# Kernel tuning notes

Hardware: AMD Instinct MI355X
Metric: run time of the kernel (lower is better)

The kernel has to match this reference:

```python
import jax, jax.numpy as jnp
import numpy as np

B = 4096
N_BLOCK = 100
N_SLOT = 300
N_YS = 1236
HID = 256
STEPS = 100
NEG = -1000.0


def _init_w(key, shape):
    # uniform(-1/sqrt(fan_in), 1/sqrt(fan_in)) like torch Linear/LSTMCell
    fan = shape[-1]
    return jax.random.uniform(key, shape, jnp.float32, -1.0, 1.0) / jnp.sqrt(jnp.float32(fan))


def setup_inputs() -> dict:
    key = jax.random.key(0)
    ks = jax.random.split(key, 16)
    to_tensor = jax.random.uniform(ks[0], (B, N_BLOCK, 5), jnp.float32)
    ti_tensor = jax.random.uniform(ks[1], (B, N_BLOCK, 5), jnp.float32)
    ys_tensor = jax.random.uniform(ks[2], (B, N_YS, 5), jnp.float32)
    # many slots are feasible, count starts at 5 so the decrement/zero-out logic is exercised.
    dims = jax.random.uniform(ks[3], (B, N_SLOT, 4), jnp.float32) * 2.0
    count = jnp.full((B, N_SLOT, 1), 5.0, jnp.float32)
    slot_info = jnp.concatenate([dims, count], axis=-1)
    params = dict(
        W1=_init_w(ks[4], (512, 1436)), b1=jnp.zeros(512, jnp.float32),
        W2=_init_w(ks[5], (512, 512)), b2=jnp.zeros(512, jnp.float32),
        W3=_init_w(ks[6], (256, 512)), b3=jnp.zeros(256, jnp.float32),
        W_fe2=_init_w(ks[7], (1, 5)), b_fe2=jnp.zeros(1, jnp.float32),
        Wih_to=_init_w(ks[8], (4 * HID, 5)), Whh_to=_init_w(ks[9], (4 * HID, HID)),
        bih_to=jnp.zeros(4 * HID, jnp.float32), bhh_to=jnp.zeros(4 * HID, jnp.float32),
        Wih_ti=_init_w(ks[10], (4 * HID, 5)), Whh_ti=_init_w(ks[11], (4 * HID, HID)),
        bih_ti=jnp.zeros(4 * HID, jnp.float32), bhh_ti=jnp.zeros(4 * HID, jnp.float32),
        Wb=_init_w(ks[12], (N_BLOCK, HID)), bb=jnp.zeros(N_BLOCK, jnp.float32),
        Ws=_init_w(ks[13], (N_SLOT, HID)), bs=jnp.zeros(N_SLOT, jnp.float32),
    )
    return {"to_tensor": to_tensor, "ti_tensor": ti_tensor, "ys_tensor": ys_tensor,
            "slot_info": slot_info, **params}


def _lstm(x, h, c, Wih, Whh, bih, bhh):
    g = x @ Wih.T + bih + h @ Whh.T + bhh  # [B, 4H]
    i, f, gg, o = jnp.split(g, 4, axis=-1)  # torch gate order: i, f, g, o
    c = jax.nn.sigmoid(f) * c + jax.nn.sigmoid(i) * jnp.tanh(gg)
    h = jax.nn.sigmoid(o) * jnp.tanh(c)
    return h, c


def reference(to_tensor, ti_tensor, ys_tensor, slot_info,
              W1, b1, W2, b2, W3, b3, W_fe2, b_fe2,
              Wih_to, Whh_to, bih_to, bhh_to,
              Wih_ti, Whh_ti, bih_ti, bhh_ti,
              Wb, bb, Ws, bs):
    state = jnp.concatenate([to_tensor, ti_tensor, ys_tensor], axis=1)  # [B,1436,5]
    x = state.transpose(0, 2, 1)                    # [B,5,1436]
    x = jax.nn.relu(x @ W1.T + b1)                  # Dropout is identity in eval mode
    x = jax.nn.relu(x @ W2.T + b2)
    x = jax.nn.relu(x @ W3.T + b3)                  # [B,5,256]
    feat_vec = (x.transpose(0, 2, 1) @ W_fe2.T + b_fe2)[..., 0]  # [B,256]

    bsz = to_tensor.shape[0]
    batch_idx = jnp.arange(bsz)
    zeros5 = jnp.zeros((bsz, 5), to_tensor.dtype)   # input_ti is never updated in the loop
    mask_to0 = to_tensor[:, :, 0] != -1.0
    mask_ti0 = ti_tensor[:, :, 0] != -1.0
    carry0 = (feat_vec, jnp.zeros((bsz, HID), jnp.float32),
              feat_vec, jnp.zeros((bsz, HID), jnp.float32),
              zeros5, mask_to0, mask_ti0, slot_info)

    def step(carry, _):
        h_to, c_to, h_ti, c_ti, inp_to, m_to, m_ti, slots = carry
        h_to, c_to = _lstm(inp_to, h_to, c_to, Wih_to, Whh_to, bih_to, bhh_to)
        # masked block logits; argmax of softmax == argmax of masked logits
        logit_b = jnp.where(m_to, h_to @ Wb.T + bb, NEG)
        sel_b = jnp.argmax(logit_b, axis=-1)                      # [B]
        inp_to = jnp.take_along_axis(to_tensor, sel_b[:, None, None], axis=1)[:, 0, :]  # [B,5]
        m_to = m_to.at[batch_idx, sel_b].set(False)
        # slot feasibility: block (l,w) must be strictly smaller than slot (l,w), slot nonempty
        slot_mask = jnp.any(inp_to[:, None, :2] >= slots[:, :, :2], axis=-1) | (slots[:, :, 0] == 0.0)
        logit_s = jnp.where(slot_mask, NEG, h_to @ Ws.T + bs)
        sel_s = jnp.argmax(logit_s, axis=-1)
        slots = slots.at[batch_idx, sel_s, 4].add(-1.0)
        slots = jnp.where((slots[:, :, 4] == 0.0)[:, :, None], 0.0, slots)
        h_ti, c_ti = _lstm(zeros5, h_ti, c_ti, Wih_ti, Whh_ti, bih_ti, bhh_ti)
        logit_bti = jnp.where(m_ti, h_ti @ Wb.T + bb, NEG)
        sel_bti = jnp.argmax(logit_bti, axis=-1)
        m_ti = m_ti.at[batch_idx, sel_bti].set(False)
        out = jnp.stack([sel_b, sel_s, sel_bti], axis=-1)         # [B,3]
        return (h_to, c_to, h_ti, c_ti, inp_to, m_to, m_ti, slots), out

    _, acts = jax.lax.scan(step, carry0, None, length=STEPS)      # [100,B,3]
    actions = acts.transpose(1, 0, 2)                             # [B,100,3]
    return state, actions
```

## Files before the change

### kernel.cpp

```cpp
#include <hip/hip_runtime.h>
#include <cstddef>

#define BATCH   4096
#define NBLK    100
#define NSLOT   300
#define NSTATE  1436
#define HID     256
#define NSTEPS  100
#define NEGV    (-1000.0f)
#define KC      384


__device__ __forceinline__ float sigf(float x) {
#pragma clang fp contract(off)
  float e = (float)exp(-(double)x);
  float d = 1.0f + e;
  return 1.0f / d;
}
__device__ __forceinline__ float tanhf32(float x) {
  return (float)tanh((double)x);
}

__device__ __forceinline__ void argmax64f(float& v, int& i) {
#pragma unroll
  for (int off = 32; off > 0; off >>= 1) {
    float v2 = __shfl_down(v, off, 64);
    int   i2 = __shfl_down(i, off, 64);
    if (v2 > v || (v2 == v && i2 < i)) { v = v2; i = i2; }
  }
  v = __shfl(v, 0, 64);
  i = __shfl(i, 0, 64);
}

__global__ __launch_bounds__(256) void concat_kernel(
    const float* __restrict__ to_t, const float* __restrict__ ti_t,
    const float* __restrict__ ys_t, float* __restrict__ state)
{
  int b = blockIdx.x;
  for (int li = threadIdx.x; li < 7180; li += 256) {
    float v = (li < 500)  ? to_t[(size_t)b * 500 + li]
            : (li < 1000) ? ti_t[(size_t)b * 500 + (li - 500)]
                          : ys_t[(size_t)b * 6180 + (li - 1000)];
    state[(size_t)b * 7180 + li] = v;
  }
}

__device__ __forceinline__ void gemm32_tile(
    const float* __restrict__ A, int lda,
    const float* __restrict__ W, int ldw,
    const float* __restrict__ bias,
    float* __restrict__ C, int ldc,
    int N, int K, int row0, int col0, bool relu)
{
#pragma clang fp contract(off)
  __shared__ float As[16][68];
  __shared__ float Ws[16][68];
  const int t = threadIdx.x;
  const int tx = t & 15, ty = t >> 4;
  const int mload = t >> 2;
  const int kq    = (t & 3) << 2;
  const int gn    = col0 + mload;
  const float* Aptr = A + (size_t)(row0 + mload) * lda + kq;
  const float* Wptr = (gn < N) ? (W + (size_t)gn * ldw + kq) : nullptr;

  float acc[4][4] = {};
  float res[4][4];
  bool first = true;
  for (int k0 = 0; k0 < K; k0 += 16) {
    if (k0 > 0 && (k0 % KC) == 0) {
#pragma unroll
      for (int i = 0; i < 4; i++)
#pragma unroll
        for (int j = 0; j < 4; j++) {
          res[i][j] = first ? acc[i][j] : (res[i][j] + acc[i][j]);
          acc[i][j] = 0.0f;
        }
      first = false;
    }
    float4 av = *(const float4*)(Aptr + k0);
    float4 wv = make_float4(0.f, 0.f, 0.f, 0.f);
    if (Wptr) wv = *(const float4*)(Wptr + k0);
    As[kq + 0][mload] = av.x; As[kq + 1][mload] = av.y;
    As[kq + 2][mload] = av.z; As[kq + 3][mload] = av.w;
    Ws[kq + 0][mload] = wv.x; Ws[kq + 1][mload] = wv.y;
    Ws[kq + 2][mload] = wv.z; Ws[kq + 3][mload] = wv.w;
    __syncthreads();
#pragma unroll
    for (int kk = 0; kk < 16; kk++) {
      float a[4], w[4];
#pragma unroll
      for (int i = 0; i < 4; i++) { a[i] = As[kk][ty * 4 + i]; w[i] = Ws[kk][tx * 4 + i]; }
#pragma unroll
      for (int i = 0; i < 4; i++)
#pragma unroll
        for (int j = 0; j < 4; j++) acc[i][j] = fmaf(a[i], w[j], acc[i][j]);
    }
    __syncthreads();
  }
#pragma unroll
  for (int i = 0; i < 4; i++)
#pragma unroll
    for (int j = 0; j < 4; j++)
      res[i][j] = first ? acc[i][j] : (res[i][j] + acc[i][j]);

#pragma unroll
  for (int i = 0; i < 4; i++) {
    size_t row = (size_t)(row0 + ty * 4 + i) * ldc;
#pragma unroll
    for (int j = 0; j < 4; j++) {
      int n = col0 + tx * 4 + j;
      if (n < N) {
        float v = res[i][j] + bias[n];
        if (relu) v = v > 0.0f ? v : 0.0f;
        C[row + n] = v;
      }
    }
  }
}

__global__ __launch_bounds__(256) void gemm32_kernel(
    const float* __restrict__ A, int lda, const float* __restrict__ W, int ldw,
    const float* __restrict__ bias, float* __restrict__ C, int ldc,
    int N, int K, int relu)
{
  gemm32_tile(A, lda, W, ldw, bias, C, ldc, N, K,
              blockIdx.y * 64, blockIdx.x * 64, relu != 0);
}

__global__ __launch_bounds__(256) void gemm1_kernel(
    const float* __restrict__ state, const float* __restrict__ W1,
    const float* __restrict__ b1, float* __restrict__ X1, int row_base)
{
#pragma clang fp contract(off)
  __shared__ float As[16][68];
  __shared__ float Ws[16][68];
  const int t = threadIdx.x;
  const int tx = t & 15, ty = t >> 4;
  const int mload = t >> 2;
  const int kq    = (t & 3) << 2;
  const int row0 = blockIdx.y * 64, col0 = blockIdx.x * 64;
  const int R = row_base + row0 + mload;
  const int b = R / 5, j = R - b * 5;
  const float* sp = state + (size_t)b * 7180 + j;
  const float* Wptr = W1 + (size_t)(col0 + mload) * NSTATE + kq;

  float acc[4][4] = {};
  float res[4][4];
  bool first = true;
  for (int k0 = 0; k0 < 1440; k0 += 16) {
    if (k0 == 384 || k0 == 768 || k0 == 1152) {
#pragma unroll
      for (int i = 0; i < 4; i++)
#pragma unroll
        for (int jj = 0; jj < 4; jj++) {
          res[i][jj] = first ? acc[i][jj] : (res[i][jj] + acc[i][jj]);
          acc[i][jj] = 0.0f;
        }
      first = false;
    }
    int n = k0 + kq;
    float a0 = (n + 0 < NSTATE) ? sp[(n + 0) * 5] : 0.0f;
    float a1 = (n + 1 < NSTATE) ? sp[(n + 1) * 5] : 0.0f;
    float a2 = (n + 2 < NSTATE) ? sp[(n + 2) * 5] : 0.0f;
    float a3 = (n + 3 < NSTATE) ? sp[(n + 3) * 5] : 0.0f;
    float4 wv = make_float4(0.f, 0.f, 0.f, 0.f);
    if (n + 3 < NSTATE) wv = *(const float4*)(Wptr + k0);
    As[kq + 0][mload] = a0; As[kq + 1][mload] = a1;
    As[kq + 2][mload] = a2; As[kq + 3][mload] = a3;
    Ws[kq + 0][mload] = wv.x; Ws[kq + 1][mload] = wv.y;
    Ws[kq + 2][mload] = wv.z; Ws[kq + 3][mload] = wv.w;
    __syncthreads();
#pragma unroll
    for (int kk = 0; kk < 16; kk++) {
      float a[4], w[4];
#pragma unroll
      for (int i = 0; i < 4; i++) { a[i] = As[kk][ty * 4 + i]; w[i] = Ws[kk][tx * 4 + i]; }
#pragma unroll
      for (int i = 0; i < 4; i++)
#pragma unroll
        for (int jj = 0; jj < 4; jj++) acc[i][jj] = fmaf(a[i], w[jj], acc[i][jj]);
    }
    __syncthreads();
  }
#pragma unroll
  for (int i = 0; i < 4; i++)
#pragma unroll
    for (int jj = 0; jj < 4; jj++)
      res[i][jj] = res[i][jj] + acc[i][jj];

#pragma unroll
  for (int i = 0; i < 4; i++) {
    size_t row = (size_t)(row0 + ty * 4 + i) * 512;
#pragma unroll
    for (int jj = 0; jj < 4; jj++) {
      int n = col0 + tx * 4 + jj;
      float v = res[i][jj] + b1[n];
      X1[row + n] = v > 0.0f ? v : 0.0f;
    }
  }
}

__global__ __launch_bounds__(256) void feat2c_kernel(
    const float* __restrict__ X3, const float* __restrict__ W_fe2,
    const float* __restrict__ b_fe2, float* __restrict__ hto,
    float* __restrict__ cto, float* __restrict__ hti, float* __restrict__ cti,
    int b_base)
{
#pragma clang fp contract(off)
  int bl = blockIdx.x, b = b_base + bl, k = threadIdx.x;
  float s = 0.0f;
#pragma unroll
  for (int j = 0; j < 5; j++)
    s = fmaf(X3[((size_t)bl * 5 + j) * 256 + k], W_fe2[j], s);
  float acc = s + b_fe2[0];
  hto[(size_t)b * 256 + k] = acc;
  hti[(size_t)b * 256 + k] = acc;
  cto[(size_t)b * 256 + k] = 0.0f;
  cti[(size_t)b * 256 + k] = 0.0f;
}

__global__ __launch_bounds__(320) void init_state_kernel(
    const float* __restrict__ to_t, const float* __restrict__ ti_t,
    const float* __restrict__ slot_info, float* __restrict__ slots,
    int* __restrict__ m_to, int* __restrict__ m_ti, float* __restrict__ inp)
{
  int b = blockIdx.x, t = threadIdx.x;
  for (int li = t; li < NSLOT * 5; li += 320)
    slots[(size_t)b * (NSLOT * 5) + li] = slot_info[(size_t)b * (NSLOT * 5) + li];
  if (t < NBLK) {
    m_to[b * 128 + t] = (to_t[(size_t)b * 500 + t * 5] != -1.0f) ? 1 : 0;
    m_ti[b * 128 + t] = (ti_t[(size_t)b * 500 + t * 5] != -1.0f) ? 1 : 0;
  }
  if (t < 8) inp[b * 8 + t] = 0.0f;
}

__global__ __launch_bounds__(256) void init_weights_kernel(
    const float* __restrict__ Wb, const float* __restrict__ bb,
    const float* __restrict__ Ws, const float* __restrict__ bs,
    float* __restrict__ Wcat, float* __restrict__ bcat)
{
  int idx = blockIdx.x * 256 + threadIdx.x;
  if (idx < 400 * 256) {
    int n = idx / 256, k = idx % 256;
    Wcat[idx] = (n < 100) ? Wb[n * 256 + k] : Ws[(n - 100) * 256 + k];
  }
  if (idx < 400) bcat[idx] = (idx < 100) ? bb[idx] : bs[idx - 100];
}

__global__ __launch_bounds__(256) void gates_kernel(
    const float* __restrict__ h, const float* __restrict__ Whh,
    const float* __restrict__ Wih, const float* __restrict__ bih,
    const float* __restrict__ bhh, const float* __restrict__ inp,
    float* __restrict__ g)
{
#pragma clang fp contract(off)
  __shared__ float As[16][68];
  __shared__ float Ws[16][68];
  const int t = threadIdx.x;
  const int tx = t & 15, ty = t >> 4;
  const int mload = t >> 2;
  const int kq    = (t & 3) << 2;
  const int row0 = blockIdx.y * 64, col0 = blockIdx.x * 64;
  const float* Aptr = h + (size_t)(row0 + mload) * 256 + kq;
  const float* Wptr = Whh + (size_t)(col0 + mload) * 256 + kq;

  float acc[4][4] = {};
  for (int k0 = 0; k0 < 256; k0 += 16) {
    float4 av = *(const float4*)(Aptr + k0);
    float4 wv = *(const float4*)(Wptr + k0);
    As[kq + 0][mload] = av.x; As[kq + 1][mload] = av.y;
    As[kq + 2][mload] = av.z; As[kq + 3][mload] = av.w;
    Ws[kq + 0][mload] = wv.x; Ws[kq + 1][mload] = wv.y;
    Ws[kq + 2][mload] = wv.z; Ws[kq + 3][mload] = wv.w;
    __syncthreads();
#pragma unroll
    for (int kk = 0; kk < 16; kk++) {
      float a[4], w[4];
#pragma unroll
      for (int i = 0; i < 4; i++) { a[i] = As[kk][ty * 4 + i]; w[i] = Ws[kk][tx * 4 + i]; }
#pragma unroll
      for (int i = 0; i < 4; i++)
#pragma unroll
        for (int j = 0; j < 4; j++) acc[i][j] = fmaf(a[i], w[j], acc[i][j]);
    }
    __syncthreads();
  }

  float wih[4][5], bihv[4], bhhv[4];
#pragma unroll
  for (int j = 0; j < 4; j++) {
    int o = col0 + tx * 4 + j;
#pragma unroll
    for (int k = 0; k < 5; k++) wih[j][k] = Wih[o * 5 + k];
    bihv[j] = bih[o];
    bhhv[j] = bhh[o];
  }
#pragma unroll
  for (int i = 0; i < 4; i++) {
    int r = row0 + ty * 4 + i;
    float xv[5];
    if (inp) {
#pragma unroll
      for (int k = 0; k < 5; k++) xv[k] = inp[r * 8 + k];
    } else {
#pragma unroll
      for (int k = 0; k < 5; k++) xv[k] = 0.0f;
    }
    size_t row = (size_t)r * 1024;
#pragma unroll
    for (int j = 0; j < 4; j++) {
      float ih = 0.0f;
#pragma unroll
      for (int k = 0; k < 5; k++) ih = fmaf(xv[k], wih[j][k], ih);
      float v1 = ih + bihv[j];
      float v2 = v1 + acc[i][j];
      float v3 = v2 + bhhv[j];
      g[row + j + tx * 4 + col0 - (tx * 4 + j) + (tx * 4 + j)] = v3;
    }
  }
}

__global__ __launch_bounds__(256) void lstm32_kernel(
    const float* __restrict__ g, float* __restrict__ h, float* __restrict__ c)
{
#pragma clang fp contract(off)
  int b = blockIdx.x, u = threadIdx.x;
  const float* gr = g + (size_t)b * 1024;
  float i_ = gr[u], f_ = gr[256 + u], gg = gr[512 + u], o_ = gr[768 + u];
  float sf = sigf(f_);
  float si = sigf(i_);
  float tg = tanhf32(gg);
  float t2 = sf * c[(size_t)b * 256 + u];
  float t5 = si * tg;
  float cc = t2 + t5;
  c[(size_t)b * 256 + u] = cc;
  float so = sigf(o_);
  float tc = tanhf32(cc);
  h[(size_t)b * 256 + u] = so * tc;
}

__global__ __launch_bounds__(256) void logits32_kernel(
    const float* __restrict__ hto, const float* __restrict__ hti,
    const float* __restrict__ Wcat, const float* __restrict__ bcat,
    const float* __restrict__ Wb, const float* __restrict__ bb,
    float* __restrict__ L)
{
  int ct = blockIdx.x;
  if (ct < 7)
    gemm32_tile(hto, 256, Wcat, 256, bcat, L, 512, 400, 256,
                blockIdx.y * 64, ct * 64, false);
  else
    gemm32_tile(hti, 256, Wb, 256, bb, L + 400, 512, 100, 256,
                blockIdx.y * 64, (ct - 7) * 64, false);
}

__global__ __launch_bounds__(64) void select32_kernel(
    const float* __restrict__ L, const float* __restrict__ to_t,
    int* __restrict__ m_to, int* __restrict__ m_ti, float* __restrict__ slots,
    float* __restrict__ inp, float* __restrict__ out_act, int step)
{
  int b = blockIdx.x, lane = threadIdx.x;
  const float* Lr = L + (size_t)b * 512;

  float bv = -3.4e38f; int bi = 0x7fffffff;
  for (int n = lane; n < NBLK; n += 64) {
    float v = m_to[b * 128 + n] ? Lr[n] : NEGV;
    if (v > bv) { bv = v; bi = n; }
  }
  argmax64f(bv, bi);
  int sel_b = bi;
  const float* blk = to_t + (size_t)b * 500 + sel_b * 5;
  float i0 = blk[0], i1 = blk[1];
  if (lane == 0) m_to[b * 128 + sel_b] = 0;
  if (lane < 5) inp[b * 8 + lane] = blk[lane];

  float sv = -3.4e38f; int si = 0x7fffffff;
  float* sl = slots + (size_t)b * (NSLOT * 5);
  for (int s = lane; s < NSLOT; s += 64) {
    float l = sl[s * 5 + 0], w = sl[s * 5 + 1];
    bool mask = (i0 >= l) || (i1 >= w) || (l == 0.0f);
    float v = mask ? NEGV : Lr[100 + s];
    if (v > sv) { sv = v; si = s; }
  }
  argmax64f(sv, si);
  int sel_s = si;
  if (lane == 0) {
    float c = sl[sel_s * 5 + 4] - 1.0f;
    if (c == 0.0f) {
      sl[sel_s * 5 + 0] = 0.f; sl[sel_s * 5 + 1] = 0.f; sl[sel_s * 5 + 2] = 0.f;
      sl[sel_s * 5 + 3] = 0.f; sl[sel_s * 5 + 4] = 0.f;
    } else {
      sl[sel_s * 5 + 4] = c;
    }
  }

  float tv = -3.4e38f; int tii = 0x7fffffff;
  for (int n = lane; n < NBLK; n += 64) {
    float v = m_ti[b * 128 + n] ? Lr[400 + n] : NEGV;
    if (v > tv) { tv = v; tii = n; }
  }
  argmax64f(tv, tii);
  if (lane == 0) {
    m_ti[b * 128 + tii] = 0;
    float* oa = out_act + (size_t)b * (NSTEPS * 3) + step * 3;
    oa[0] = (float)sel_b; oa[1] = (float)sel_s; oa[2] = (float)tii;
  }
}

extern "C" void kernel_launch(void* const* d_in, const int* in_sizes, int n_in,
                              void* d_out, int out_size, void* d_ws, size_t ws_size,
                              hipStream_t stream) {
  (void)in_sizes; (void)n_in; (void)out_size; (void)ws_size;
  const float* to_t   = (const float*)d_in[0];
  const float* ti_t   = (const float*)d_in[1];
  const float* ys_t   = (const float*)d_in[2];
  const float* slot_i = (const float*)d_in[3];
  const float* W1 = (const float*)d_in[4];  const float* b1 = (const float*)d_in[5];
  const float* W2 = (const float*)d_in[6];  const float* b2 = (const float*)d_in[7];
  const float* W3 = (const float*)d_in[8];  const float* b3 = (const float*)d_in[9];
  const float* W_fe2 = (const float*)d_in[10]; const float* b_fe2 = (const float*)d_in[11];
  const float* Wih_to = (const float*)d_in[12]; const float* Whh_to = (const float*)d_in[13];
  const float* bih_to = (const float*)d_in[14]; const float* bhh_to = (const float*)d_in[15];
  const float* Wih_ti = (const float*)d_in[16]; const float* Whh_ti = (const float*)d_in[17];
  const float* bih_ti = (const float*)d_in[18]; const float* bhh_ti = (const float*)d_in[19];
  const float* Wb = (const float*)d_in[20]; const float* bb = (const float*)d_in[21];
  const float* Ws = (const float*)d_in[22]; const float* bs = (const float*)d_in[23];

  float* outf      = (float*)d_out;
  float* state_out = outf;
  float* out_act   = outf + (size_t)BATCH * NSTATE * 5;

  float* ws = (float*)d_ws;
  float* X1 = ws;
  float* X2 = ws + 1310720;
  float* X3 = ws + 2621440;
  float* g  = ws;
  float* Lb = ws + 4194304;
  float* hto = ws + 6291456;
  float* hti = ws + 7340032;
  float* cto = ws + 8388608;
  float* cti = ws + 9437184;
  float* slots = ws + 10485760;
  int*   m_to  = (int*)(ws + 16629760);
  int*   m_ti  = (int*)(ws + 17154048);
  float* inp_buf = ws + 17678336;
  float* Wcat  = ws + 17711104;
  float* bcat  = ws + 17813504;

  concat_kernel<<<dim3(BATCH), 256, 0, stream>>>(to_t, ti_t, ys_t, state_out);
  init_state_kernel<<<dim3(BATCH), 320, 0, stream>>>(to_t, ti_t, slot_i, slots,
                                                     m_to, m_ti, inp_buf);
  init_weights_kernel<<<dim3(400), 256, 0, stream>>>(Wb, bb, Ws, bs, Wcat, bcat);

  for (int c = 0; c < 8; c++) {
    int rb = c * 2560, b0 = c * 512;
    gemm1_kernel<<<dim3(8, 40), 256, 0, stream>>>(state_out, W1, b1, X1, rb);
    gemm32_kernel<<<dim3(8, 40), 256, 0, stream>>>(X1, 512, W2, 512, b2,
                                                   X2, 512, 512, 512, 1);
    gemm32_kernel<<<dim3(4, 40), 256, 0, stream>>>(X2, 512, W3, 512, b3,
                                                   X3, 256, 256, 512, 1);
    feat2c_kernel<<<dim3(512), 256, 0, stream>>>(X3, W_fe2, b_fe2,
                                                 hto, cto, hti, cti, b0);
  }

  for (int s = 0; s < NSTEPS; s++) {
    gates_kernel<<<dim3(16, 64), 256, 0, stream>>>(hto, Whh_to, Wih_to,
                                                   bih_to, bhh_to, inp_buf, g);
    lstm32_kernel<<<dim3(BATCH), 256, 0, stream>>>(g, hto, cto);
    gates_kernel<<<dim3(16, 64), 256, 0, stream>>>(hti, Whh_ti, Wih_ti,
                                                   bih_ti, bhh_ti, nullptr, g);
    lstm32_kernel<<<dim3(BATCH), 256, 0, stream>>>(g, hti, cti);
    logits32_kernel<<<dim3(9, 64), 256, 0, stream>>>(hto, hti, Wcat, bcat, Wb, bb, Lb);
    select32_kernel<<<dim3(BATCH), 64, 0, stream>>>(Lb, to_t, m_to, m_ti, slots,
                                                    inp_buf, out_act, s);
  }
}
```

Measured before the change: 15.49 ms.

## Fuse LSTM gate GEMM with cell update and batch both LSTMs per launch

Replaces the separate gate GEMM and elementwise LSTM kernels with one kernel. Each block computes all four gates for a slice of 32 hidden units by interleaving i/f/g/o weight rows, then applies the cell update in registers, so the [B,1024] gate buffer is never written to or read back from global memory. Both LSTMs run in a single launch via blockIdx.z, and the hidden state is double-buffered so the new h can be written while other blocks still read the old one. Tiles grow to 128x128 with an 8x8 per-thread accumulator, which raises register pressure and may lower occupancy.

```diff
diff --git a/kernel.cpp b/kernel.cpp
--- a/kernel.cpp
+++ b/kernel.cpp
@@ -247,96 +247,125 @@
   if (idx < 400) bcat[idx] = (idx < 100) ? bb[idx] : bs[idx - 100];
 }
 
-__global__ __launch_bounds__(256) void gates_kernel(
-    const float* __restrict__ h, const float* __restrict__ Whh,
-    const float* __restrict__ Wih, const float* __restrict__ bih,
-    const float* __restrict__ bhh, const float* __restrict__ inp,
-    float* __restrict__ g)
+__global__ __launch_bounds__(256) void gates_lstm_kernel(
+    const float* __restrict__ hto_old, const float* __restrict__ hti_old,
+    float* __restrict__ hto_new, float* __restrict__ hti_new,
+    float* __restrict__ cto, float* __restrict__ cti,
+    const float* __restrict__ Whh_to, const float* __restrict__ Whh_ti,
+    const float* __restrict__ Wih_to, const float* __restrict__ Wih_ti,
+    const float* __restrict__ bih_to, const float* __restrict__ bih_ti,
+    const float* __restrict__ bhh_to, const float* __restrict__ bhh_ti,
+    const float* __restrict__ inp)
 {
 #pragma clang fp contract(off)
-  __shared__ float As[16][68];
-  __shared__ float Ws[16][68];
-  const int t = threadIdx.x;
+  const int z = blockIdx.z;
+  const float* h_old = z ? hti_old : hto_old;
+  float* h_new = z ? hti_new : hto_new;
+  float* cbuf  = z ? cti : cto;
+  const float* Whh  = z ? Whh_ti : Whh_to;
+  const float* Wih  = z ? Wih_ti : Wih_to;
+  const float* bihp = z ? bih_ti : bih_to;
+  const float* bhhp = z ? bhh_ti : bhh_to;
+
+  const int u0   = blockIdx.x * 32;
+  const int row0 = blockIdx.y * 128;
+  const int t  = threadIdx.x;
   const int tx = t & 15, ty = t >> 4;
-  const int mload = t >> 2;
-  const int kq    = (t & 3) << 2;
-  const int row0 = blockIdx.y * 64, col0 = blockIdx.x * 64;
-  const float* Aptr = h + (size_t)(row0 + mload) * 256 + kq;
-  const float* Wptr = Whh + (size_t)(col0 + mload) * 256 + kq;
-
-  float acc[4][4] = {};
+
+  __shared__ float As[16][132];
+  __shared__ float Bs[16][132];
+
+  const int q  = t >> 2;
+  const int kq = (t & 3) << 2;
+  const float* aptr[2];
+  const float* wptr[2];
+  int colp[2];
+#pragma unroll
+  for (int pass = 0; pass < 2; pass++) {
+    const int p = pass * 64 + q;
+    colp[pass] = p;
+    aptr[pass] = h_old + (size_t)(row0 + p) * 256 + kq;
+    const int m = p >> 4;
+    const int o = (m & 3) * 256 + u0 + ((m >> 2) << 4) + (p & 15);
+    wptr[pass] = Whh + (size_t)o * 256 + kq;
+  }
+
+  float acc[8][8];
+#pragma unroll
+  for (int i = 0; i < 8; i++)
+#pragma unroll
+    for (int m = 0; m < 8; m++) acc[i][m] = 0.0f;
+
   for (int k0 = 0; k0 < 256; k0 += 16) {
-    float4 av = *(const float4*)(Aptr + k0);
-    float4 wv = *(const float4*)(Wptr + k0);
-    As[kq + 0][mload] = av.x; As[kq + 1][mload] = av.y;
-    As[kq + 2][mload] = av.z; As[kq + 3][mload] = av.w;
-    Ws[kq + 0][mload] = wv.x; Ws[kq + 1][mload] = wv.y;
-    Ws[kq + 2][mload] = wv.z; Ws[kq + 3][mload] = wv.w;
+    float4 av0 = *(const float4*)(aptr[0] + k0);
+    float4 av1 = *(const float4*)(aptr[1] + k0);
+    float4 wv0 = *(const float4*)(wptr[0] + k0);
+    float4 wv1 = *(const float4*)(wptr[1] + k0);
+    if (k0) __syncthreads();
+    As[kq + 0][colp[0]] = av0.x; As[kq + 1][colp[0]] = av0.y;
+    As[kq + 2][colp[0]] = av0.z; As[kq + 3][colp[0]] = av0.w;
+    As[kq + 0][colp[1]] = av1.x; As[kq + 1][colp[1]] = av1.y;
+    As[kq + 2][colp[1]] = av1.z; As[kq + 3][colp[1]] = av1.w;
+    Bs[kq + 0][colp[0]] = wv0.x; Bs[kq + 1][colp[0]] = wv0.y;
+    Bs[kq + 2][colp[0]] = wv0.z; Bs[kq + 3][colp[0]] = wv0.w;
+    Bs[kq + 0][colp[1]] = wv1.x; Bs[kq + 1][colp[1]] = wv1.y;
+    Bs[kq + 2][colp[1]] = wv1.z; Bs[kq + 3][colp[1]] = wv1.w;
     __syncthreads();
 #pragma unroll
     for (int kk = 0; kk < 16; kk++) {
-      float a[4], w[4];
-#pragma unroll
-      for (int i = 0; i < 4; i++) { a[i] = As[kk][ty * 4 + i]; w[i] = Ws[kk][tx * 4 + i]; }
-#pragma unroll
-      for (int i = 0; i < 4; i++)
-#pragma unroll
-        for (int j = 0; j < 4; j++) acc[i][j] = fmaf(a[i], w[j], acc[i][j]);
-    }
-    __syncthreads();
-  }
-
-  float wih[4][5], bihv[4], bhhv[4];
-#pragma unroll
-  for (int j = 0; j < 4; j++) {
-    int o = col0 + tx * 4 + j;
-#pragma unroll
-    for (int k = 0; k < 5; k++) wih[j][k] = Wih[o * 5 + k];
-    bihv[j] = bih[o];
-    bhhv[j] = bhh[o];
-  }
-#pragma unroll
-  for (int i = 0; i < 4; i++) {
-    int r = row0 + ty * 4 + i;
-    float xv[5];
-    if (inp) {
-#pragma unroll
-      for (int k = 0; k < 5; k++) xv[k] = inp[r * 8 + k];
-    } else {
-#pragma unroll
-      for (int k = 0; k < 5; k++) xv[k] = 0.0f;
-    }
-    size_t row = (size_t)r * 1024;
-#pragma unroll
-    for (int j = 0; j < 4; j++) {
-      float ih = 0.0f;
-#pragma unroll
-      for (int k = 0; k < 5; k++) ih = fmaf(xv[k], wih[j][k], ih);
-      float v1 = ih + bihv[j];
-      float v2 = v1 + acc[i][j];
-      float v3 = v2 + bhhv[j];
-      g[row + j + tx * 4 + col0 - (tx * 4 + j) + (tx * 4 + j)] = v3;
-    }
-  }
-}
-
-__global__ __launch_bounds__(256) void lstm32_kernel(
-    const float* __restrict__ g, float* __restrict__ h, float* __restrict__ c)
-{
-#pragma clang fp contract(off)
-  int b = blockIdx.x, u = threadIdx.x;
-  const float* gr = g + (size_t)b * 1024;
-  float i_ = gr[u], f_ = gr[256 + u], gg = gr[512 + u], o_ = gr[768 + u];
-  float sf = sigf(f_);
-  float si = sigf(i_);
-  float tg = tanhf32(gg);
-  float t2 = sf * c[(size_t)b * 256 + u];
-  float t5 = si * tg;
-  float cc = t2 + t5;
-  c[(size_t)b * 256 + u] = cc;
-  float so = sigf(o_);
-  float tc = tanhf32(cc);
-  h[(size_t)b * 256 + u] = so * tc;
+      float a[8], w[8];
+#pragma unroll
+      for (int i = 0; i < 8; i++) a[i] = As[kk][ty * 8 + i];
+#pragma unroll
+      for (int m = 0; m < 8; m++) w[m] = Bs[kk][m * 16 + tx];
+#pragma unroll
+      for (int i = 0; i < 8; i++)
+#pragma unroll
+        for (int m = 0; m < 8; m++)
+          acc[i][m] = fmaf(a[i], w[m], acc[i][m]);
+    }
+  }
+
+  const int urow = row0 + ty * 8;
+#pragma unroll
+  for (int i = 0; i < 8; i++) {
+    const int r = urow + i;
+    float x0 = 0.f, x1 = 0.f, x2 = 0.f, x3 = 0.f, x4 = 0.f;
+    if (!z) {
+      const float* xp = inp + r * 8;
+      x0 = xp[0]; x1 = xp[1]; x2 = xp[2]; x3 = xp[3]; x4 = xp[4];
+    }
+#pragma unroll
+    for (int uu = 0; uu < 2; uu++) {
+      const int u = u0 + uu * 16 + tx;
+      float v[4];
+#pragma unroll
+      for (int g = 0; g < 4; g++) {
+        const int o = g * 256 + u;
+        const float* wp = Wih + o * 5;
+        float ih = 0.0f;
+        ih = fmaf(x0, wp[0], ih);
+        ih = fmaf(x1, wp[1], ih);
+        ih = fmaf(x2, wp[2], ih);
+        ih = fmaf(x3, wp[3], ih);
+        ih = fmaf(x4, wp[4], ih);
+        float v1 = ih + bihp[o];
+        float v2 = v1 + acc[i][uu * 4 + g];
+        v[g] = v2 + bhhp[o];
+      }
+      const size_t ci = (size_t)r * 256 + u;
+      float sf = sigf(v[1]);
+      float si = sigf(v[0]);
+      float tg = tanhf32(v[2]);
+      float t2 = sf * cbuf[ci];
+      float t5 = si * tg;
+      float cc = t2 + t5;
+      cbuf[ci] = cc;
+      float so = sigf(v[3]);
+      float tc = tanhf32(cc);
+      h_new[ci] = so * tc;
+    }
+  }
 }
 
 __global__ __launch_bounds__(256) void logits32_kernel(
@@ -434,18 +463,19 @@
   float* X1 = ws;
   float* X2 = ws + 1310720;
   float* X3 = ws + 2621440;
-  float* g  = ws;
-  float* Lb = ws + 4194304;
-  float* hto = ws + 6291456;
-  float* hti = ws + 7340032;
-  float* cto = ws + 8388608;
-  float* cti = ws + 9437184;
-  float* slots = ws + 10485760;
-  int*   m_to  = (int*)(ws + 16629760);
-  int*   m_ti  = (int*)(ws + 17154048);
-  float* inp_buf = ws + 17678336;
-  float* Wcat  = ws + 17711104;
-  float* bcat  = ws + 17813504;
+  float* Lb = ws;
+  float* hto0 = ws + 3276800;
+  float* hto1 = ws + 4325376;
+  float* hti0 = ws + 5373952;
+  float* hti1 = ws + 6422528;
+  float* cto  = ws + 7471104;
+  float* cti  = ws + 8519680;
+  float* slots = ws + 9568256;
+  int*   m_to  = (int*)(ws + 15712256);
+  int*   m_ti  = (int*)(ws + 16236544);
+  float* inp_buf = ws + 16760832;
+  float* Wcat  = ws + 16793600;
+  float* bcat  = ws + 16896000;
 
   concat_kernel<<<dim3(BATCH), 256, 0, stream>>>(to_t, ti_t, ys_t, state_out);
   init_state_kernel<<<dim3(BATCH), 320, 0, stream>>>(to_t, ti_t, slot_i, slots,
@@ -460,18 +490,22 @@
     gemm32_kernel<<<dim3(4, 40), 256, 0, stream>>>(X2, 512, W3, 512, b3,
                                                    X3, 256, 256, 512, 1);
     feat2c_kernel<<<dim3(512), 256, 0, stream>>>(X3, W_fe2, b_fe2,
-                                                 hto, cto, hti, cti, b0);
-  }
-
+                                                 hto0, cto, hti0, cti, b0);
+  }
+
+  float* hto_o = hto0; float* hto_n = hto1;
+  float* hti_o = hti0; float* hti_n = hti1;
   for (int s = 0; s < NSTEPS; s++) {
-    gates_kernel<<<dim3(16, 64), 256, 0, stream>>>(hto, Whh_to, Wih_to,
-                                                   bih_to, bhh_to, inp_buf, g);
-    lstm32_kernel<<<dim3(BATCH), 256, 0, stream>>>(g, hto, cto);
-    gates_kernel<<<dim3(16, 64), 256, 0, stream>>>(hti, Whh_ti, Wih_ti,
-                                                   bih_ti, bhh_ti, nullptr, g);
-    lstm32_kernel<<<dim3(BATCH), 256, 0, stream>>>(g, hti, cti);
-    logits32_kernel<<<dim3(9, 64), 256, 0, stream>>>(hto, hti, Wcat, bcat, Wb, bb, Lb);
+    gates_lstm_kernel<<<dim3(8, 32, 2), 256, 0, stream>>>(
+        hto_o, hti_o, hto_n, hti_n, cto, cti,
+        Whh_to, Whh_ti, Wih_to, Wih_ti,
+        bih_to, bih_ti, bhh_to, bhh_ti, inp_buf);
+    logits32_kernel<<<dim3(9, 64), 256, 0, stream>>>(hto_n, hti_n, Wcat, bcat,
+                                                     Wb, bb, Lb);
     select32_kernel<<<dim3(BATCH), 64, 0, stream>>>(Lb, to_t, m_to, m_ti, slots,
                                                     inp_buf, out_act, s);
-  }
-}
+    float* tmp;
+    tmp = hto_o; hto_o = hto_n; hto_n = tmp;
+    tmp = hti_o; hti_o = hti_n; hti_n = tmp;
+  }
+}
```

After: 15.22 ms. About the same (-1.7%).
